# Performance work log

Hardware: AMD Instinct MI355X
Metric: run time of the kernel (lower is better)

## Reference

```python
import jax, jax.numpy as jnp
import numpy as np

BLK = 128            # weight_block_size for w8a16 blockwise dequant
H = 1024             # hidden_size
I = 512              # moe_intermediate_size
E = 64               # n_routed_experts
T = 512              # tokens (seq_len)
K = 6                # num_experts_per_tok
G = 8                # n_group
TG = 3               # topk_group
NSH = 2              # n_shared_experts
I2 = I * NSH         # shared expert intermediate size
ROUTED_SCALE = 2.5
NORM_TOPK = True


def dq(w_int8, scale, blk=BLK):
    """Blockwise w8a16 dequant: w [..., M, N] int8, scale [..., M/blk, N/blk] f32."""
    *lead, M, N = w_int8.shape
    w = w_int8.astype(scale.dtype).reshape(*lead, M // blk, blk, N // blk, blk)
    return (w * scale[..., :, None, :, None]).reshape(*lead, M, N)


def setup_inputs() -> dict:
    key = jax.random.key(0)
    ks = jax.random.split(key, 16)
    ri = lambda k, shp: jax.random.randint(k, shp, -8, 8, dtype=jnp.int8)
    rs = lambda k, shp: jax.random.uniform(k, shp, minval=0.01, maxval=0.03, dtype=jnp.float32)
    return {
        "x": jax.random.normal(ks[0], (T, H), jnp.float32),
        "gate_w": jax.random.normal(ks[1], (E, H), jnp.float32) * 0.02,  # router gate [E,H]
        "wg": ri(ks[2], (E, I, H)),  "sg": rs(ks[3], (E, I // BLK, H // BLK)),
        "wu": ri(ks[4], (E, I, H)),  "su": rs(ks[5], (E, I // BLK, H // BLK)),
        "wd": ri(ks[6], (E, I, H)),  "sd": rs(ks[7], (E, I // BLK, H // BLK)),  # down, transposed layout [I,H]
        "sh_wg": ri(ks[8], (I2, H)),  "sh_sg": rs(ks[9], (I2 // BLK, H // BLK)),
        "sh_wu": ri(ks[10], (I2, H)), "sh_su": rs(ks[11], (I2 // BLK, H // BLK)),
        "sh_wd": ri(ks[12], (I2, H)), "sh_sd": rs(ks[13], (I2 // BLK, H // BLK)),
    }


def _moe(x, gate_w, wg, sg, wu, su, wd, sd, sh_wg, sh_sg, sh_wu, sh_su, sh_wd, sh_sd):
    Tn = x.shape[0]
    # --- router: sigmoid scoring + group-limited top-k ---
    scores = jax.nn.sigmoid(x @ gate_w.T)                       # [T, E]
    gsz = E // G
    group_scores = scores.reshape(Tn, G, gsz).max(axis=-1)      # [T, G]
    _, gidx = jax.lax.top_k(group_scores, TG)                   # [T, TG]
    gmask = jax.nn.one_hot(gidx, G, dtype=scores.dtype).sum(1)  # [T, G]
    emask = jnp.repeat(gmask, gsz, axis=-1)                     # [T, E]
    masked = jnp.where(emask > 0, scores, -jnp.inf)
    w, idx = jax.lax.top_k(masked, K)                           # [T, K]
    if NORM_TOPK:
        w = w / (w.sum(-1, keepdims=True) + 1e-20)
    w = w * ROUTED_SCALE
    # per-token combine weights over experts
    comb = (jax.nn.one_hot(idx, E, dtype=x.dtype) * w[:, :, None]).sum(1)  # [T, E]

    # --- routed experts: dequantized silu-gated MLPs, masked dense combine ---
    Wg, Wu, Wd = dq(wg, sg), dq(wu, su), dq(wd, sd)             # [E, I, H]
    g = jnp.einsum('th,eih->eti', x, Wg)                        # [E, T, I]
    u = jnp.einsum('th,eih->eti', x, Wu)
    hmid = jax.nn.silu(g) * u
    y = jnp.einsum('eti,eih->eth', hmid, Wd)                    # [E, T, H]
    routed = jnp.einsum('eth,te->th', y, comb)                  # [T, H]

    # --- shared experts MLP ---
    Sg, Su, Sd = dq(sh_wg, sh_sg), dq(sh_wu, sh_su), dq(sh_wd, sh_sd)
    shared = (jax.nn.silu(x @ Sg.T) * (x @ Su.T)) @ Sd          # [T, H]
    return routed + shared


def reference(x, gate_w, wg, sg, wu, su, wd, sd, sh_wg, sh_sg, sh_wu, sh_su, sh_wd, sh_sd):
    return _moe(x, gate_w, wg, sg, wu, su, wd, sd,
                sh_wg, sh_sg, sh_wu, sh_su, sh_wd, sh_sd)
```

## Files before the change

### kernel.cpp

```cpp
#include <hip/hip_runtime.h>
#include <math.h>
#include <stdint.h>

#define T_   512
#define H_   1024
#define I_   512
#define E_   64
#define K_   6
#define G_   8
#define TG_  3
#define EB_  72

typedef _Float16 h8 __attribute__((ext_vector_type(8)));
typedef _Float16 h4v __attribute__((ext_vector_type(4)));
typedef float    f4 __attribute__((ext_vector_type(4)));

__global__ __launch_bounds__(64) void router_k(
    const float* __restrict__ x, const float* __restrict__ gw,
    int* __restrict__ cnt, int* __restrict__ tlist, float* __restrict__ wlist)
{
  const int t   = blockIdx.x;
  const int tid = threadIdx.x;
  __shared__ float sx[H_];
  __shared__ float sc[E_];

  for (int h4 = tid; h4 < H_/4; h4 += 64)
    ((float4*)sx)[h4] = ((const float4*)(x + (size_t)t*H_))[h4];
  __syncthreads();

  const float* wr = gw + (size_t)tid * H_;
  float acc = 0.f;
  for (int h = 0; h < H_; h += 4) {
    float4 xv = *(const float4*)(sx + h);
    float4 wv = *(const float4*)(wr + h);
    acc = fmaf(xv.x, wv.x, acc); acc = fmaf(xv.y, wv.y, acc);
    acc = fmaf(xv.z, wv.z, acc); acc = fmaf(xv.w, wv.w, acc);
  }
  sc[tid] = 1.f / (1.f + expf(-acc));
  __syncthreads();

  if (tid == 0) {
    float gs[G_];
    #pragma unroll
    for (int g = 0; g < G_; g++) {
      float m = sc[g*8];
      #pragma unroll
      for (int j = 1; j < 8; j++) m = fmaxf(m, sc[g*8+j]);
      gs[g] = m;
    }
    unsigned gp = 0;
    for (int r = 0; r < TG_; r++) {
      int best = 0; float bv = -1e30f;
      for (int g = 0; g < G_; g++)
        if (!((gp >> g) & 1) && gs[g] > bv) { bv = gs[g]; best = g; }
      gp |= 1u << best;
    }
    int   eidx[K_]; float ew[K_];
    unsigned long long em = 0ull;
    float wsum = 0.f;
    for (int r = 0; r < K_; r++) {
      int best = 0; float bv = -1e30f;
      for (int e = 0; e < E_; e++) {
        if (!((gp >> (e >> 3)) & 1)) continue;
        if ((em >> e) & 1ull) continue;
        if (sc[e] > bv) { bv = sc[e]; best = e; }
      }
      em |= 1ull << best; eidx[r] = best; ew[r] = bv; wsum += bv;
    }
    const float inv = 2.5f / (wsum + 1e-20f);
    for (int r = 0; r < K_; r++) {
      int e = eidx[r];
      int pos = atomicAdd(&cnt[e], 1);
      tlist[e*T_ + pos] = (t << 13) | (t*K_ + r);
      wlist[e*T_ + pos] = ew[r] * inv;
    }
  }
}

__global__ void pseudo_init_k(int* cnt, int* tlist, float* wlist) {
  int s = blockIdx.x*256 + threadIdx.x;
  if (s == 0) { cnt[64] = T_; cnt[65] = T_; }
  if (s < 1024) {
    int e = 64 + (s >> 9);
    int t = s & 511;
    tlist[e*T_ + t] = (t << 13) | (3072 + s);
    wlist[e*T_ + t] = 1.0f;
  }
}

__global__ __launch_bounds__(256) void xh_prep_k(
    const float* __restrict__ x, _Float16* __restrict__ xh)
{
  int i = blockIdx.x*256 + threadIdx.x;
  float4 v = ((const float4*)x)[i];
  h4v o = { (_Float16)v.x, (_Float16)v.y, (_Float16)v.z, (_Float16)v.w };
  *(h4v*)(xh + (size_t)i*4) = o;
}

__device__ __forceinline__ void eb_decode(int eb, const int* cnt,
                                          int& e, int& lo, int& hi) {
  if (eb < E_) { e = eb; lo = 0; hi = cnt[e]; }
  else { int q = (eb - E_) & 3; e = E_ + ((eb - E_) >> 2); lo = q*128; hi = lo + 128; }
}

__device__ __forceinline__ h8 bfrag(const int* __restrict__ p, float s) {
  int4 a = *(const int4*)(p);
  int4 b = *(const int4*)(p + 4);
  union { _Float16 f[8]; h8 v; } t;
  t.f[0]=(_Float16)((float)a.x*s); t.f[1]=(_Float16)((float)a.y*s);
  t.f[2]=(_Float16)((float)a.z*s); t.f[3]=(_Float16)((float)a.w*s);
  t.f[4]=(_Float16)((float)b.x*s); t.f[5]=(_Float16)((float)b.y*s);
  t.f[6]=(_Float16)((float)b.z*s); t.f[7]=(_Float16)((float)b.w*s);
  return t.v;
}

__global__ __launch_bounds__(256) void gateup_k(
    const _Float16* __restrict__ xh,
    const int* __restrict__ wg, const float* __restrict__ sg,
    const int* __restrict__ wu, const float* __restrict__ su,
    const int* __restrict__ shwg, const float* __restrict__ shsg,
    const int* __restrict__ shwu, const float* __restrict__ shsu,
    const int* __restrict__ cnt, const int* __restrict__ tlist,
    const float* __restrict__ wlist,
    _Float16* __restrict__ hmid)
{
  const int ic = blockIdx.x;
  const int eb = blockIdx.y;
  int e, lo, hi;
  eb_decode(eb, cnt, e, lo, hi);
  if (hi <= lo) return;

  const int tid  = threadIdx.x;
  const int lane = tid & 63;
  const int wv   = tid >> 6;
  const int mr   = lane & 15;
  const int quad = lane >> 4;

  const int *wgb, *wub; const float *sgp, *sup; int sib;
  if (e < E_) {
    wgb = wg + (size_t)e*I_*H_;  wub = wu + (size_t)e*I_*H_;
    sgp = sg + e*32;  sup = su + e*32;  sib = ic >> 1;
  } else {
    int hf = e - E_;
    wgb = shwg + (size_t)hf*512*H_;  wub = shwu + (size_t)hf*512*H_;
    sgp = shsg;  sup = shsu;  sib = hf*4 + (ic >> 1);
  }
  float scg[8], scu[8];
  #pragma unroll
  for (int hb = 0; hb < 8; hb++) { scg[hb] = sgp[sib*8+hb]; scu[hb] = sup[sib*8+hb]; }

  const int r0 = ic*64 + wv*16 + mr;
  const int* gp = wgb + (size_t)r0*H_;
  const int* up = wub + (size_t)r0*H_;

  __shared__ int   stok[64];
  __shared__ int   srow[64];
  __shared__ float swt[64];

  for (int base = lo; base < hi; base += 64) {
    __syncthreads();
    if (tid < 64) {
      int slot = base + tid;
      if (slot < hi) {
        int ent = tlist[e*T_ + slot];
        stok[tid] = ent >> 13; srow[tid] = ent & 8191; swt[tid] = wlist[e*T_ + slot];
      } else { stok[tid] = -1; srow[tid] = 0; swt[tid] = 0.f; }
    }
    __syncthreads();

    const _Float16* ax[4];
    #pragma unroll
    for (int mt = 0; mt < 4; mt++) {
      int tok = stok[mt*16 + mr];
      ax[mt] = xh + (size_t)(tok < 0 ? 0 : tok) * H_ + quad*8;
    }

    f4 accg[4], accu[4];
    #pragma unroll
    for (int mt = 0; mt < 4; mt++) { accg[mt] = (f4){0.f,0.f,0.f,0.f}; accu[mt] = accg[mt]; }

    #pragma unroll 4
    for (int kt = 0; kt < 32; kt++) {
      const int k0 = kt*32 + quad*8;
      const float sg_ = scg[kt>>2], su_ = scu[kt>>2];
      h8 bg = bfrag(gp + k0, sg_);
      h8 bu = bfrag(up + k0, su_);
      #pragma unroll
      for (int mt = 0; mt < 4; mt++) {
        h8 av = *(const h8*)(ax[mt] + kt*32);
        accg[mt] = __builtin_amdgcn_mfma_f32_16x16x32_f16(av, bg, accg[mt], 0,0,0);
        accu[mt] = __builtin_amdgcn_mfma_f32_16x16x32_f16(av, bu, accu[mt], 0,0,0);
      }
    }

    const int icol = ic*64 + wv*16 + mr;
    #pragma unroll
    for (int mt = 0; mt < 4; mt++) {
      #pragma unroll
      for (int r = 0; r < 4; r++) {
        int sl = mt*16 + quad*4 + r;
        if (stok[sl] >= 0) {
          float g = accg[mt][r];
          float m = g / (1.f + expf(-g)) * accu[mt][r] * swt[sl];
          hmid[(size_t)srow[sl]*I_ + icol] = (_Float16)m;
        }
      }
    }
  }
}

__global__ __launch_bounds__(256) void down_k(
    const int* __restrict__ wd, const float* __restrict__ sd,
    const int* __restrict__ shwd, const float* __restrict__ shsd,
    const int* __restrict__ cnt, const int* __restrict__ tlist,
    const _Float16* __restrict__ hmid, float* __restrict__ out)
{
  const int hc = blockIdx.x;
  const int eb = blockIdx.y;
  int e, lo, hi;
  eb_decode(eb, cnt, e, lo, hi);
  if (hi <= lo) return;

  const int tid  = threadIdx.x;
  const int lane = tid & 63;
  const int wv   = tid >> 6;
  const int mr   = lane & 15;
  const int quad = lane >> 4;

  const int* wb; const float* sdp; int sib0;
  if (e < E_) { wb = wd + (size_t)e*I_*H_;        sdp = sd + e*32;  sib0 = 0; }
  else { int hf = e - E_; wb = shwd + (size_t)hf*512*H_; sdp = shsd; sib0 = hf*4; }
  float scd[4];
  #pragma unroll
  for (int ib = 0; ib < 4; ib++) scd[ib] = sdp[(sib0+ib)*8 + hc];

  const int hcol0 = hc*128 + wv*32 + mr;
  const int* bcol0 = wb + hcol0;

  __shared__ int stok[64];
  __shared__ int srow[64];

  for (int base = lo; base < hi; base += 64) {
    __syncthreads();
    if (tid < 64) {
      int slot = base + tid;
      if (slot < hi) {
        int ent = tlist[e*T_ + slot];
        stok[tid] = ent >> 13; srow[tid] = ent & 8191;
      } else { stok[tid] = -1; srow[tid] = 0; }
    }
    __syncthreads();

    const _Float16* ap[4];
    #pragma unroll
    for (int mt = 0; mt < 4; mt++)
      ap[mt] = hmid + (size_t)srow[mt*16 + mr]*I_ + quad*8;

    f4 a0[4], a1[4];
    #pragma unroll
    for (int mt = 0; mt < 4; mt++) { a0[mt] = (f4){0.f,0.f,0.f,0.f}; a1[mt] = a0[mt]; }

    #pragma unroll 2
    for (int kt = 0; kt < 16; kt++) {
      const float s = scd[kt>>2];
      const size_t ib0 = (size_t)(kt*32 + quad*8) * H_;
      union { _Float16 f[8]; h8 v; } b0, b1;
      #pragma unroll
      for (int j = 0; j < 8; j++) {
        b0.f[j] = (_Float16)((float)bcol0[ib0 + (size_t)j*H_     ] * s);
        b1.f[j] = (_Float16)((float)bcol0[ib0 + (size_t)j*H_ + 16] * s);
      }
      #pragma unroll
      for (int mt = 0; mt < 4; mt++) {
        h8 av = *(const h8*)(ap[mt] + kt*32);
        a0[mt] = __builtin_amdgcn_mfma_f32_16x16x32_f16(av, b0.v, a0[mt], 0,0,0);
        a1[mt] = __builtin_amdgcn_mfma_f32_16x16x32_f16(av, b1.v, a1[mt], 0,0,0);
      }
    }

    #pragma unroll
    for (int mt = 0; mt < 4; mt++) {
      #pragma unroll
      for (int p = 0; p < 2; p++) {
        f4 av2 = (p == 0) ? a0[mt] : a1[mt];
        const int hcol = hcol0 + p*16;
        #pragma unroll
        for (int r = 0; r < 4; r++) {
          int sl = mt*16 + quad*4 + r;
          int t = stok[sl];
          if (t >= 0) atomicAdd(out + (size_t)t*H_ + hcol, av2[r]);
        }
      }
    }
  }
}

extern "C" void kernel_launch(void* const* d_in, const int* in_sizes, int n_in,
                              void* d_out, int out_size, void* d_ws, size_t ws_size,
                              hipStream_t stream) {
  (void)in_sizes; (void)n_in; (void)ws_size;
  const float* x    = (const float*)d_in[0];
  const float* gw   = (const float*)d_in[1];
  const int*   wg   = (const int*  )d_in[2];
  const float* sg   = (const float*)d_in[3];
  const int*   wu   = (const int*  )d_in[4];
  const float* su   = (const float*)d_in[5];
  const int*   wd   = (const int*  )d_in[6];
  const float* sd   = (const float*)d_in[7];
  const int*   shwg = (const int*  )d_in[8];
  const float* shsg = (const float*)d_in[9];
  const int*   shwu = (const int*  )d_in[10];
  const float* shsu = (const float*)d_in[11];
  const int*   shwd = (const int*  )d_in[12];
  const float* shsd = (const float*)d_in[13];
  float* out = (float*)d_out;

  char* ws = (char*)d_ws;
  int*      cnt   = (int*     ) ws;
  int*      tlist = (int*     )(ws + 1024);
  float*    wlist = (float*   )(ws + 1024 + 66*T_*4);
  _Float16* hmid  = (_Float16*)(ws + 1024 + 2*66*T_*4);
  _Float16* xh    = (_Float16*)(ws + 1024 + 2*66*T_*4 + 4096*I_*2);

  hipMemsetAsync(cnt, 0, 1024, stream);
  hipMemsetAsync(d_out, 0, (size_t)out_size * sizeof(float), stream);
  xh_prep_k<<<T_*H_/1024, 256, 0, stream>>>(x, xh);
  router_k<<<T_, 64, 0, stream>>>(x, gw, cnt, tlist, wlist);
  pseudo_init_k<<<4, 256, 0, stream>>>(cnt, tlist, wlist);
  gateup_k<<<dim3(8, EB_), 256, 0, stream>>>(xh, wg, sg, wu, su,
                                             shwg, shsg, shwu, shsu,
                                             cnt, tlist, wlist, hmid);
  down_k<<<dim3(8, EB_), 256, 0, stream>>>(wd, sd, shwd, shsd,
                                           cnt, tlist, hmid, out);
}
```

Baseline: 541.1 us.

## Double-buffer int weight tiles in LDS via async global_load_lds in gate/up and down

```diff
diff --git a/kernel.cpp b/kernel.cpp
--- a/kernel.cpp
+++ b/kernel.cpp
@@ -9,7 +9,7 @@
 #define K_   6
 #define G_   8
 #define TG_  3
-#define EB_  72
+#define EB_  80
 
 typedef _Float16 h8 __attribute__((ext_vector_type(8)));
 typedef _Float16 h4v __attribute__((ext_vector_type(4)));
@@ -100,12 +100,16 @@
 __device__ __forceinline__ void eb_decode(int eb, const int* cnt,
                                           int& e, int& lo, int& hi) {
   if (eb < E_) { e = eb; lo = 0; hi = cnt[e]; }
-  else { int q = (eb - E_) & 3; e = E_ + ((eb - E_) >> 2); lo = q*128; hi = lo + 128; }
-}
-
-__device__ __forceinline__ h8 bfrag(const int* __restrict__ p, float s) {
-  int4 a = *(const int4*)(p);
-  int4 b = *(const int4*)(p + 4);
+  else { int q = (eb - E_) & 7; e = E_ + ((eb - E_) >> 3); lo = q*64; hi = lo + 64; }
+}
+
+__device__ __forceinline__ void gld16(const int* g, void* l) {
+  __builtin_amdgcn_global_load_lds(
+      (const __attribute__((address_space(1))) void*)g,
+      (__attribute__((address_space(3))) void*)l, 16, 0, 0);
+}
+
+__device__ __forceinline__ h8 cvt8(int4 a, int4 b, float s) {
   union { _Float16 f[8]; h8 v; } t;
   t.f[0]=(_Float16)((float)a.x*s); t.f[1]=(_Float16)((float)a.y*s);
   t.f[2]=(_Float16)((float)a.z*s); t.f[3]=(_Float16)((float)a.w*s);
@@ -114,7 +118,13 @@
   return t.v;
 }
 
-__global__ __launch_bounds__(256) void gateup_k(
+#define PIPE_SYNC() do { \
+    asm volatile("s_waitcnt vmcnt(0)" ::: "memory"); \
+    __builtin_amdgcn_s_barrier(); \
+    __builtin_amdgcn_sched_barrier(0); } while (0)
+
+#define NKT_G 16
+__global__ __launch_bounds__(256, 2) void gateup_k(
     const _Float16* __restrict__ xh,
     const int* __restrict__ wg, const float* __restrict__ sg,
     const int* __restrict__ wu, const float* __restrict__ su,
@@ -145,17 +155,27 @@
     wgb = shwg + (size_t)hf*512*H_;  wub = shwu + (size_t)hf*512*H_;
     sgp = shsg;  sup = shsu;  sib = hf*4 + (ic >> 1);
   }
-  float scg[8], scu[8];
-  #pragma unroll
-  for (int hb = 0; hb < 8; hb++) { scg[hb] = sgp[sib*8+hb]; scu[hb] = sup[sib*8+hb]; }
-
-  const int r0 = ic*64 + wv*16 + mr;
-  const int* gp = wgb + (size_t)r0*H_;
-  const int* up = wub + (size_t)r0*H_;
-
+  const int r0base = ic*64;
+
+  __shared__ int   ldsw[2][2][4096];
   __shared__ int   stok[64];
   __shared__ int   srow[64];
   __shared__ float swt[64];
+
+  auto stage = [&](int buf, int kt) {
+    const int k0 = kt * 64;
+    #pragma unroll
+    for (int i = 0; i < 4; i++) {
+      const int rl  = i*16 + wv*4 + (lane >> 4);
+      const int csw = (lane & 15) ^ (rl & 7);
+      const size_t go = (size_t)(r0base + rl)*H_ + k0 + csw*4;
+      gld16(wgb + go, &ldsw[buf][0][(i*16 + wv*4)*64]);
+      gld16(wub + go, &ldsw[buf][1][(i*16 + wv*4)*64]);
+    }
+  };
+
+  const int rr = wv*16 + mr;
+  const int sw = rr & 7;
 
   for (int base = lo; base < hi; base += 64) {
     __syncthreads();
@@ -179,21 +199,43 @@
     #pragma unroll
     for (int mt = 0; mt < 4; mt++) { accg[mt] = (f4){0.f,0.f,0.f,0.f}; accu[mt] = accg[mt]; }
 
-    #pragma unroll 4
-    for (int kt = 0; kt < 32; kt++) {
-      const int k0 = kt*32 + quad*8;
-      const float sg_ = scg[kt>>2], su_ = scu[kt>>2];
-      h8 bg = bfrag(gp + k0, sg_);
-      h8 bu = bfrag(up + k0, su_);
+    stage(0, 0);
+    PIPE_SYNC();
+
+    int cur = 0;
+    for (int kt = 0; kt < NKT_G; kt++) {
+      h8 avv[4][2];
       #pragma unroll
       for (int mt = 0; mt < 4; mt++) {
-        h8 av = *(const h8*)(ax[mt] + kt*32);
-        accg[mt] = __builtin_amdgcn_mfma_f32_16x16x32_f16(av, bg, accg[mt], 0,0,0);
-        accu[mt] = __builtin_amdgcn_mfma_f32_16x16x32_f16(av, bu, accu[mt], 0,0,0);
-      }
-    }
-
-    const int icol = ic*64 + wv*16 + mr;
+        avv[mt][0] = *(const h8*)(ax[mt] + kt*64);
+        avv[mt][1] = *(const h8*)(ax[mt] + kt*64 + 32);
+      }
+      __builtin_amdgcn_sched_barrier(0);
+      if (kt < NKT_G-1) stage(cur ^ 1, kt + 1);
+
+      const float sg_ = sgp[sib*8 + (kt >> 1)];
+      const float su_ = sup[sib*8 + (kt >> 1)];
+      const int* lg = &ldsw[cur][0][0];
+      const int* lu = &ldsw[cur][1][0];
+      #pragma unroll
+      for (int ktl = 0; ktl < 2; ktl++) {
+        const int c0 = ktl*8 + quad*2;
+        int4 g0 = *(const int4*)(lg + rr*64 + (( c0   ) ^ sw)*4);
+        int4 g1 = *(const int4*)(lg + rr*64 + (((c0+1)) ^ sw)*4);
+        int4 u0 = *(const int4*)(lu + rr*64 + (( c0   ) ^ sw)*4);
+        int4 u1 = *(const int4*)(lu + rr*64 + (((c0+1)) ^ sw)*4);
+        h8 bg = cvt8(g0, g1, sg_);
+        h8 bu = cvt8(u0, u1, su_);
+        #pragma unroll
+        for (int mt = 0; mt < 4; mt++) {
+          accg[mt] = __builtin_amdgcn_mfma_f32_16x16x32_f16(avv[mt][ktl], bg, accg[mt], 0,0,0);
+          accu[mt] = __builtin_amdgcn_mfma_f32_16x16x32_f16(avv[mt][ktl], bu, accu[mt], 0,0,0);
+        }
+      }
+      if (kt < NKT_G-1) { PIPE_SYNC(); cur ^= 1; }
+    }
+
+    const int icol = ic*64 + rr;
     #pragma unroll
     for (int mt = 0; mt < 4; mt++) {
       #pragma unroll
@@ -209,7 +251,8 @@
   }
 }
 
-__global__ __launch_bounds__(256) void down_k(
+#define NKT_D 8
+__global__ __launch_bounds__(256, 2) void down_k(
     const int* __restrict__ wd, const float* __restrict__ sd,
     const int* __restrict__ shwd, const float* __restrict__ shsd,
     const int* __restrict__ cnt, const int* __restrict__ tlist,
@@ -230,15 +273,28 @@
   const int* wb; const float* sdp; int sib0;
   if (e < E_) { wb = wd + (size_t)e*I_*H_;        sdp = sd + e*32;  sib0 = 0; }
   else { int hf = e - E_; wb = shwd + (size_t)hf*512*H_; sdp = shsd; sib0 = hf*4; }
-  float scd[4];
-  #pragma unroll
-  for (int ib = 0; ib < 4; ib++) scd[ib] = sdp[(sib0+ib)*8 + hc];
-
-  const int hcol0 = hc*128 + wv*32 + mr;
-  const int* bcol0 = wb + hcol0;
-
+
+  __shared__ int ldsd[2][8192];
   __shared__ int stok[64];
   __shared__ int srow[64];
+
+  auto stage = [&](int buf, int kt) {
+    const int i0 = kt*64;
+    #pragma unroll
+    for (int s = 0; s < 8; s++) {
+      const int rl  = s*8 + wv*2 + (lane >> 5);
+      const int csw = (lane & 31) ^ (((rl >> 3) & 1) << 2);
+      gld16(wb + (size_t)(i0 + rl)*H_ + hc*128 + csw*4,
+            &ldsd[buf][(s*8 + wv*2)*128]);
+    }
+  };
+
+  const int hcol0 = hc*128 + wv*32 + mr;
+  const int swd   = (quad & 1) << 2;
+  const int cd0   = wv*32 + mr;
+  const int cd1   = cd0 + 16;
+  const int off0  = (((cd0 >> 2) ^ swd) << 2) + (cd0 & 3);
+  const int off1  = (((cd1 >> 2) ^ swd) << 2) + (cd1 & 3);
 
   for (int base = lo; base < hi; base += 64) {
     __syncthreads();
@@ -260,22 +316,38 @@
     #pragma unroll
     for (int mt = 0; mt < 4; mt++) { a0[mt] = (f4){0.f,0.f,0.f,0.f}; a1[mt] = a0[mt]; }
 
-    #pragma unroll 2
-    for (int kt = 0; kt < 16; kt++) {
-      const float s = scd[kt>>2];
-      const size_t ib0 = (size_t)(kt*32 + quad*8) * H_;
-      union { _Float16 f[8]; h8 v; } b0, b1;
-      #pragma unroll
-      for (int j = 0; j < 8; j++) {
-        b0.f[j] = (_Float16)((float)bcol0[ib0 + (size_t)j*H_     ] * s);
-        b1.f[j] = (_Float16)((float)bcol0[ib0 + (size_t)j*H_ + 16] * s);
-      }
+    stage(0, 0);
+    PIPE_SYNC();
+
+    int cur = 0;
+    for (int kt = 0; kt < NKT_D; kt++) {
+      h8 avv[4][2];
       #pragma unroll
       for (int mt = 0; mt < 4; mt++) {
-        h8 av = *(const h8*)(ap[mt] + kt*32);
-        a0[mt] = __builtin_amdgcn_mfma_f32_16x16x32_f16(av, b0.v, a0[mt], 0,0,0);
-        a1[mt] = __builtin_amdgcn_mfma_f32_16x16x32_f16(av, b1.v, a1[mt], 0,0,0);
-      }
+        avv[mt][0] = *(const h8*)(ap[mt] + kt*64);
+        avv[mt][1] = *(const h8*)(ap[mt] + kt*64 + 32);
+      }
+      __builtin_amdgcn_sched_barrier(0);
+      if (kt < NKT_D-1) stage(cur ^ 1, kt + 1);
+
+      const float s = sdp[(sib0 + (kt >> 1))*8 + hc];
+      const int* lb = &ldsd[cur][0];
+      #pragma unroll
+      for (int ktl = 0; ktl < 2; ktl++) {
+        union { _Float16 f[8]; h8 v; } b0, b1;
+        #pragma unroll
+        for (int j = 0; j < 8; j++) {
+          const int r = ktl*32 + quad*8 + j;
+          b0.f[j] = (_Float16)((float)lb[r*128 + off0] * s);
+          b1.f[j] = (_Float16)((float)lb[r*128 + off1] * s);
+        }
+        #pragma unroll
+        for (int mt = 0; mt < 4; mt++) {
+          a0[mt] = __builtin_amdgcn_mfma_f32_16x16x32_f16(avv[mt][ktl], b0.v, a0[mt], 0,0,0);
+          a1[mt] = __builtin_amdgcn_mfma_f32_16x16x32_f16(avv[mt][ktl], b1.v, a1[mt], 0,0,0);
+        }
+      }
+      if (kt < NKT_D-1) { PIPE_SYNC(); cur ^= 1; }
     }
 
     #pragma unroll
```

Measured after the change: 517.2 us. 4.4% less time.

## Stage dequantized weights through LDS with software pipelining and replace atomics with scratch combine

Applied to the files above, without the earlier changes.

```diff
diff --git a/kernel.cpp b/kernel.cpp
--- a/kernel.cpp
+++ b/kernel.cpp
@@ -9,7 +9,7 @@
 #define K_   6
 #define G_   8
 #define TG_  3
-#define EB_  72
+#define EB_  80
 
 typedef _Float16 h8 __attribute__((ext_vector_type(8)));
 typedef _Float16 h4v __attribute__((ext_vector_type(4)));
@@ -100,21 +100,53 @@
 __device__ __forceinline__ void eb_decode(int eb, const int* cnt,
                                           int& e, int& lo, int& hi) {
   if (eb < E_) { e = eb; lo = 0; hi = cnt[e]; }
-  else { int q = (eb - E_) & 3; e = E_ + ((eb - E_) >> 2); lo = q*128; hi = lo + 128; }
-}
-
-__device__ __forceinline__ h8 bfrag(const int* __restrict__ p, float s) {
-  int4 a = *(const int4*)(p);
-  int4 b = *(const int4*)(p + 4);
+  else { int q = (eb - E_) & 7; e = E_ + ((eb - E_) >> 3); lo = q*64; hi = lo + 64; }
+}
+
+__device__ __forceinline__ h8 cvt8i(int4 a, int4 b) {
   union { _Float16 f[8]; h8 v; } t;
-  t.f[0]=(_Float16)((float)a.x*s); t.f[1]=(_Float16)((float)a.y*s);
-  t.f[2]=(_Float16)((float)a.z*s); t.f[3]=(_Float16)((float)a.w*s);
-  t.f[4]=(_Float16)((float)b.x*s); t.f[5]=(_Float16)((float)b.y*s);
-  t.f[6]=(_Float16)((float)b.z*s); t.f[7]=(_Float16)((float)b.w*s);
+  t.f[0]=(_Float16)a.x; t.f[1]=(_Float16)a.y; t.f[2]=(_Float16)a.z; t.f[3]=(_Float16)a.w;
+  t.f[4]=(_Float16)b.x; t.f[5]=(_Float16)b.y; t.f[6]=(_Float16)b.z; t.f[7]=(_Float16)b.w;
   return t.v;
 }
 
-__global__ __launch_bounds__(256) void gateup_k(
+#define NKT_G 16
+
+#define GU_STEP(KT, WN)                                                       \
+  do {                                                                        \
+    asm volatile("s_waitcnt vmcnt(" #WN ") lgkmcnt(0)" ::: "memory");         \
+    __builtin_amdgcn_sched_barrier(0);                                        \
+    __builtin_amdgcn_s_barrier();                                             \
+    if ((KT) + 1 < NKT_G)                                                     \
+      *(h8*)(wdst + (((KT)+1)&1)*4608) =                                      \
+          cvt8i(Wr[((KT)+1)%3][0], Wr[((KT)+1)%3][1]);                        \
+    if ((KT) + 3 < NKT_G) {                                                   \
+      Wr[((KT)+3)%3][0] = *(const int4*)(wsrc + ((KT)+3)*64);                 \
+      Wr[((KT)+3)%3][1] = *(const int4*)(wsrc + ((KT)+3)*64 + 4);             \
+    }                                                                         \
+    {                                                                         \
+      const char* tb = tb0 + (((KT)&1))*4608;                                 \
+      h8 bg0 = *(const h8*)(tb);                                              \
+      h8 bg1 = *(const h8*)(tb + 64);                                         \
+      h8 bu0 = *(const h8*)(tb + 2304);                                       \
+      h8 bu1 = *(const h8*)(tb + 2304 + 64);                                  \
+      if (((KT)&1) == 0) { partg = (f4){0.f,0.f,0.f,0.f}; partu = partg; }    \
+      partg = __builtin_amdgcn_mfma_f32_16x16x32_f16(Ar[(KT)%3][0], bg0, partg, 0,0,0); \
+      partg = __builtin_amdgcn_mfma_f32_16x16x32_f16(Ar[(KT)%3][1], bg1, partg, 0,0,0); \
+      partu = __builtin_amdgcn_mfma_f32_16x16x32_f16(Ar[(KT)%3][0], bu0, partu, 0,0,0); \
+      partu = __builtin_amdgcn_mfma_f32_16x16x32_f16(Ar[(KT)%3][1], bu1, partu, 0,0,0); \
+      if (((KT)&1) == 1) {                                                    \
+        totg += partg * sgv[(KT)>>1];                                         \
+        totu += partu * suv[(KT)>>1];                                         \
+      }                                                                       \
+    }                                                                         \
+    if ((KT) + 3 < NKT_G) {                                                   \
+      Ar[((KT)+3)%3][0] = *(const h8*)(ax + ((KT)+3)*64);                     \
+      Ar[((KT)+3)%3][1] = *(const h8*)(ax + ((KT)+3)*64 + 32);                \
+    }                                                                         \
+  } while (0)
+
+__global__ __launch_bounds__(256, 6) void gateup_k(
     const _Float16* __restrict__ xh,
     const int* __restrict__ wg, const float* __restrict__ sg,
     const int* __restrict__ wu, const float* __restrict__ su,
@@ -139,23 +171,28 @@
   const int *wgb, *wub; const float *sgp, *sup; int sib;
   if (e < E_) {
     wgb = wg + (size_t)e*I_*H_;  wub = wu + (size_t)e*I_*H_;
-    sgp = sg + e*32;  sup = su + e*32;  sib = ic >> 1;
+    sgp = sg + e*32;  sup = su + e*32;  sib = ic >> 3;
   } else {
     int hf = e - E_;
     wgb = shwg + (size_t)hf*512*H_;  wub = shwu + (size_t)hf*512*H_;
-    sgp = shsg;  sup = shsu;  sib = hf*4 + (ic >> 1);
-  }
-  float scg[8], scu[8];
+    sgp = shsg;  sup = shsu;  sib = hf*4 + (ic >> 3);
+  }
+  float sgv[8], suv[8];
   #pragma unroll
-  for (int hb = 0; hb < 8; hb++) { scg[hb] = sgp[sib*8+hb]; scu[hb] = sup[sib*8+hb]; }
-
-  const int r0 = ic*64 + wv*16 + mr;
-  const int* gp = wgb + (size_t)r0*H_;
-  const int* up = wub + (size_t)r0*H_;
-
-  __shared__ int   stok[64];
-  __shared__ int   srow[64];
-  __shared__ float swt[64];
+  for (int b = 0; b < 8; b++) { sgv[b] = sgp[sib*8+b]; suv[b] = sup[sib*8+b]; }
+
+  __shared__ _Float16 tile[2][2][16][72];
+  __shared__ int stok[64]; __shared__ int srw[64]; __shared__ float swt[64];
+  char* tilebytes = (char*)&tile[0][0][0][0];
+
+  const int smat = wv >> 1;
+  const int srow = (wv & 1)*8 + (lane >> 3);
+  const int* wsrc = (smat ? wub : wgb) + (size_t)(ic*16 + srow)*H_ + (lane & 7)*8;
+  char* wdst = tilebytes + smat*2304 + srow*144 + (lane & 7)*16;
+  const char* tb0 = tilebytes + mr*144 + quad*16;
+
+  int4 Wr[3][2];
+  h8   Ar[3][2];
 
   for (int base = lo; base < hi; base += 64) {
     __syncthreads();
@@ -163,57 +200,98 @@
       int slot = base + tid;
       if (slot < hi) {
         int ent = tlist[e*T_ + slot];
-        stok[tid] = ent >> 13; srow[tid] = ent & 8191; swt[tid] = wlist[e*T_ + slot];
-      } else { stok[tid] = -1; srow[tid] = 0; swt[tid] = 0.f; }
+        stok[tid] = ent >> 13; srw[tid] = ent & 8191; swt[tid] = wlist[e*T_ + slot];
+      } else { stok[tid] = -1; srw[tid] = 0; swt[tid] = 0.f; }
     }
     __syncthreads();
 
-    const _Float16* ax[4];
+    int tk = stok[wv*16 + mr]; if (tk < 0) tk = 0;
+    const _Float16* ax = xh + (size_t)tk*H_ + quad*8;
+
+    f4 totg = (f4){0.f,0.f,0.f,0.f}, totu = totg, partg = totg, partu = totg;
+
+    Wr[0][0] = *(const int4*)(wsrc);       Wr[0][1] = *(const int4*)(wsrc + 4);
+    Ar[0][0] = *(const h8*)(ax);           Ar[0][1] = *(const h8*)(ax + 32);
+    Wr[1][0] = *(const int4*)(wsrc + 64);  Wr[1][1] = *(const int4*)(wsrc + 68);
+    Ar[1][0] = *(const h8*)(ax + 64);      Ar[1][1] = *(const h8*)(ax + 96);
+    Wr[2][0] = *(const int4*)(wsrc + 128); Wr[2][1] = *(const int4*)(wsrc + 132);
+    Ar[2][0] = *(const h8*)(ax + 128);     Ar[2][1] = *(const h8*)(ax + 160);
+    *(h8*)(wdst) = cvt8i(Wr[0][0], Wr[0][1]);
+
+    GU_STEP(0,6);  GU_STEP(1,6);  GU_STEP(2,6);  GU_STEP(3,6);
+    GU_STEP(4,6);  GU_STEP(5,6);  GU_STEP(6,6);  GU_STEP(7,6);
+    GU_STEP(8,6);  GU_STEP(9,6);  GU_STEP(10,6); GU_STEP(11,6);
+    GU_STEP(12,6); GU_STEP(13,6); GU_STEP(14,2); GU_STEP(15,0);
+
+    const int icol = ic*16 + mr;
     #pragma unroll
-    for (int mt = 0; mt < 4; mt++) {
-      int tok = stok[mt*16 + mr];
-      ax[mt] = xh + (size_t)(tok < 0 ? 0 : tok) * H_ + quad*8;
-    }
-
-    f4 accg[4], accu[4];
-    #pragma unroll
-    for (int mt = 0; mt < 4; mt++) { accg[mt] = (f4){0.f,0.f,0.f,0.f}; accu[mt] = accg[mt]; }
-
-    #pragma unroll 4
-    for (int kt = 0; kt < 32; kt++) {
-      const int k0 = kt*32 + quad*8;
-      const float sg_ = scg[kt>>2], su_ = scu[kt>>2];
-      h8 bg = bfrag(gp + k0, sg_);
-      h8 bu = bfrag(up + k0, su_);
-      #pragma unroll
-      for (int mt = 0; mt < 4; mt++) {
-        h8 av = *(const h8*)(ax[mt] + kt*32);
-        accg[mt] = __builtin_amdgcn_mfma_f32_16x16x32_f16(av, bg, accg[mt], 0,0,0);
-        accu[mt] = __builtin_amdgcn_mfma_f32_16x16x32_f16(av, bu, accu[mt], 0,0,0);
+    for (int r = 0; r < 4; r++) {
+      int sl = wv*16 + quad*4 + r;
+      if (stok[sl] >= 0) {
+        float g = totg[r];
+        float m = g / (1.f + expf(-g)) * totu[r] * swt[sl];
+        hmid[(size_t)srw[sl]*I_ + icol] = (_Float16)m;
       }
     }
-
-    const int icol = ic*64 + wv*16 + mr;
-    #pragma unroll
-    for (int mt = 0; mt < 4; mt++) {
-      #pragma unroll
-      for (int r = 0; r < 4; r++) {
-        int sl = mt*16 + quad*4 + r;
-        if (stok[sl] >= 0) {
-          float g = accg[mt][r];
-          float m = g / (1.f + expf(-g)) * accu[mt][r] * swt[sl];
-          hmid[(size_t)srow[sl]*I_ + icol] = (_Float16)m;
-        }
-      }
-    }
-  }
-}
-
-__global__ __launch_bounds__(256) void down_k(
+  }
+}
+#undef GU_STEP
+
+#define NKT_D 8
+
+#define DN_LDW(S, KT)                                                         \
+  do {                                                                        \
+    Wr[S][0] = *(const int2*)(dsrc + (size_t)((KT)*64 + 0)*H_);               \
+    Wr[S][1] = *(const int2*)(dsrc + (size_t)((KT)*64 + 1)*H_);               \
+    Wr[S][2] = *(const int2*)(dsrc + (size_t)((KT)*64 + 2)*H_);               \
+    Wr[S][3] = *(const int2*)(dsrc + (size_t)((KT)*64 + 3)*H_);               \
+  } while (0)
+
+#define DN_WRITE(S, BUF)                                                      \
+  do {                                                                        \
+    union { _Float16 f[4]; h4v v; } v0, v1;                                   \
+    v0.f[0]=(_Float16)Wr[S][0].x; v0.f[1]=(_Float16)Wr[S][1].x;               \
+    v0.f[2]=(_Float16)Wr[S][2].x; v0.f[3]=(_Float16)Wr[S][3].x;               \
+    v1.f[0]=(_Float16)Wr[S][0].y; v1.f[1]=(_Float16)Wr[S][1].y;               \
+    v1.f[2]=(_Float16)Wr[S][2].y; v1.f[3]=(_Float16)Wr[S][3].y;               \
+    *(h4v*)(ddst + (BUF)*4608)       = v0.v;                                  \
+    *(h4v*)(ddst + (BUF)*4608 + 144) = v1.v;                                  \
+  } while (0)
+
+#define DN_STEP(KT, WN)                                                       \
+  do {                                                                        \
+    asm volatile("s_waitcnt vmcnt(" #WN ") lgkmcnt(0)" ::: "memory");         \
+    __builtin_amdgcn_sched_barrier(0);                                        \
+    __builtin_amdgcn_s_barrier();                                             \
+    if ((KT) + 1 < NKT_D) DN_WRITE(((KT)+1)%3, ((KT)+1)&1);                   \
+    if ((KT) + 3 < NKT_D) DN_LDW(((KT)+3)%3, (KT)+3);                         \
+    {                                                                         \
+      const char* tb = tb0 + (((KT)&1))*4608;                                 \
+      h8 b00 = *(const h8*)(tb);                                              \
+      h8 b01 = *(const h8*)(tb + 64);                                         \
+      h8 b10 = *(const h8*)(tb + 2304);                                       \
+      h8 b11 = *(const h8*)(tb + 2304 + 64);                                  \
+      if (((KT)&1) == 0) { part0 = (f4){0.f,0.f,0.f,0.f}; part1 = part0; }    \
+      part0 = __builtin_amdgcn_mfma_f32_16x16x32_f16(Ar[(KT)%3][0], b00, part0, 0,0,0); \
+      part0 = __builtin_amdgcn_mfma_f32_16x16x32_f16(Ar[(KT)%3][1], b01, part0, 0,0,0); \
+      part1 = __builtin_amdgcn_mfma_f32_16x16x32_f16(Ar[(KT)%3][0], b10, part1, 0,0,0); \
+      part1 = __builtin_amdgcn_mfma_f32_16x16x32_f16(Ar[(KT)%3][1], b11, part1, 0,0,0); \
+      if (((KT)&1) == 1) {                                                    \
+        tot0 += part0 * sdv[(KT)>>1];                                         \
+        tot1 += part1 * sdv[(KT)>>1];                                         \
+      }                                                                       \
+    }                                                                         \
+    if ((KT) + 3 < NKT_D) {                                                   \
+      Ar[((KT)+3)%3][0] = *(const h8*)(ap + ((KT)+3)*64);                     \
+      Ar[((KT)+3)%3][1] = *(const h8*)(ap + ((KT)+3)*64 + 32);                \
+    }                                                                         \
+  } while (0)
+
+__global__ __launch_bounds__(256, 6) void down_k(
     const int* __restrict__ wd, const float* __restrict__ sd,
     const int* __restrict__ shwd, const float* __restrict__ shsd,
     const int* __restrict__ cnt, const int* __restrict__ tlist,
-    const _Float16* __restrict__ hmid, float* __restrict__ out)
+    const _Float16* __restrict__ hmid, float* __restrict__ scr)
 {
   const int hc = blockIdx.x;
   const int eb = blockIdx.y;
@@ -230,15 +308,21 @@
   const int* wb; const float* sdp; int sib0;
   if (e < E_) { wb = wd + (size_t)e*I_*H_;        sdp = sd + e*32;  sib0 = 0; }
   else { int hf = e - E_; wb = shwd + (size_t)hf*512*H_; sdp = shsd; sib0 = hf*4; }
-  float scd[4];
+  float sdv[4];
   #pragma unroll
-  for (int ib = 0; ib < 4; ib++) scd[ib] = sdp[(sib0+ib)*8 + hc];
-
-  const int hcol0 = hc*128 + wv*32 + mr;
-  const int* bcol0 = wb + hcol0;
-
-  __shared__ int stok[64];
-  __shared__ int srow[64];
+  for (int ib = 0; ib < 4; ib++) sdv[ib] = sdp[(sib0+ib)*8 + (hc >> 2)];
+
+  __shared__ _Float16 tile[2][32][72];
+  __shared__ int stok[64]; __shared__ int srw[64];
+  char* tilebytes = (char*)&tile[0][0][0];
+
+  const int rg = lane >> 4;
+  const int* dsrc = wb + (size_t)(wv*16 + rg*4)*H_ + hc*32 + (lane & 15)*2;
+  char* ddst = tilebytes + ((lane & 15)*2)*144 + (wv*16 + rg*4)*2;
+  const char* tb0 = tilebytes + mr*144 + quad*16;
+
+  int2 Wr[3][4];
+  h8   Ar[3][2];
 
   for (int base = lo; base < hi; base += 64) {
     __syncthreads();
@@ -246,59 +330,64 @@
       int slot = base + tid;
       if (slot < hi) {
         int ent = tlist[e*T_ + slot];
-        stok[tid] = ent >> 13; srow[tid] = ent & 8191;
-      } else { stok[tid] = -1; srow[tid] = 0; }
+        stok[tid] = ent >> 13; srw[tid] = ent & 8191;
+      } else { stok[tid] = -1; srw[tid] = 0; }
     }
     __syncthreads();
 
-    const _Float16* ap[4];
+    const _Float16* ap = hmid + (size_t)srw[wv*16 + mr]*I_ + quad*8;
+
+    f4 tot0 = (f4){0.f,0.f,0.f,0.f}, tot1 = tot0, part0 = tot0, part1 = tot0;
+
+    DN_LDW(0, 0);
+    Ar[0][0] = *(const h8*)(ap);        Ar[0][1] = *(const h8*)(ap + 32);
+    DN_LDW(1, 1);
+    Ar[1][0] = *(const h8*)(ap + 64);   Ar[1][1] = *(const h8*)(ap + 96);
+    DN_LDW(2, 2);
+    Ar[2][0] = *(const h8*)(ap + 128);  Ar[2][1] = *(const h8*)(ap + 160);
+    DN_WRITE(0, 0);
+
+    DN_STEP(0,6); DN_STEP(1,6); DN_STEP(2,6); DN_STEP(3,6);
+    DN_STEP(4,6); DN_STEP(5,6); DN_STEP(6,2); DN_STEP(7,0);
+
     #pragma unroll
-    for (int mt = 0; mt < 4; mt++)
-      ap[mt] = hmid + (size_t)srow[mt*16 + mr]*I_ + quad*8;
-
-    f4 a0[4], a1[4];
-    #pragma unroll
-    for (int mt = 0; mt < 4; mt++) { a0[mt] = (f4){0.f,0.f,0.f,0.f}; a1[mt] = a0[mt]; }
-
-    #pragma unroll 2
-    for (int kt = 0; kt < 16; kt++) {
-      const float s = scd[kt>>2];
-      const size_t ib0 = (size_t)(kt*32 + quad*8) * H_;
-      union { _Float16 f[8]; h8 v; } b0, b1;
-      #pragma unroll
-      for (int j = 0; j < 8; j++) {
-        b0.f[j] = (_Float16)((float)bcol0[ib0 + (size_t)j*H_     ] * s);
-        b1.f[j] = (_Float16)((float)bcol0[ib0 + (size_t)j*H_ + 16] * s);
+    for (int r = 0; r < 4; r++) {
+      int sl = wv*16 + quad*4 + r;
+      if (stok[sl] >= 0) {
+        int t  = stok[sl];
+        int sr = srw[sl];
+        int rank = (sr < 3072) ? (sr - t*6) : (6 + ((sr - 3072) >> 9));
+        float* dst = scr + (size_t)(t*8 + rank)*H_ + hc*32 + mr;
+        dst[0]  = tot0[r];
+        dst[16] = tot1[r];
       }
-      #pragma unroll
-      for (int mt = 0; mt < 4; mt++) {
-        h8 av = *(const h8*)(ap[mt] + kt*32);
-        a0[mt] = __builtin_amdgcn_mfma_f32_16x16x32_f16(av, b0.v, a0[mt], 0,0,0);
-        a1[mt] = __builtin_amdgcn_mfma_f32_16x16x32_f16(av, b1.v, a1[mt], 0,0,0);
-      }
-    }
-
-    #pragma unroll
-    for (int mt = 0; mt < 4; mt++) {
-      #pragma unroll
-      for (int p = 0; p < 2; p++) {
-        f4 av2 = (p == 0) ? a0[mt] : a1[mt];
-        const int hcol = hcol0 + p*16;
-        #pragma unroll
-        for (int r = 0; r < 4; r++) {
-          int sl = mt*16 + quad*4 + r;
-          int t = stok[sl];
-          if (t >= 0) atomicAdd(out + (size_t)t*H_ + hcol, av2[r]);
-        }
-      }
-    }
-  }
+    }
+  }
+}
+#undef DN_STEP
+#undef DN_WRITE
+#undef DN_LDW
+
+__global__ __launch_bounds__(256) void combine_k(
+    const float* __restrict__ scr, float* __restrict__ out)
+{
+  int i = blockIdx.x*256 + threadIdx.x;
+  int t = i >> 8;
+  int c = i & 255;
+  const float4* base = (const float4*)(scr + (size_t)t*8*H_) + c;
+  float4 s = base[0];
+  #pragma unroll
+  for (int r = 1; r < 8; r++) {
+    float4 v = base[(size_t)r*(H_/4)];
+    s.x += v.x; s.y += v.y; s.z += v.z; s.w += v.w;
+  }
+  ((float4*)out)[i] = s;
 }
 
 extern "C" void kernel_launch(void* const* d_in, const int* in_sizes, int n_in,
                               void* d_out, int out_size, void* d_ws, size_t ws_size,
                               hipStream_t stream) {
-  (void)in_sizes; (void)n_in; (void)ws_size;
+  (void)in_sizes; (void)n_in; (void)ws_size; (void)out_size;
   const float* x    = (const float*)d_in[0];
   const float* gw   = (const float*)d_in[1];
   const int*   wg   = (const int*  )d_in[2];
@@ -321,15 +410,16 @@
   float*    wlist = (float*   )(ws + 1024 + 66*T_*4);
   _Float16* hmid  = (_Float16*)(ws + 1024 + 2*66*T_*4);
   _Float16* xh    = (_Float16*)(ws + 1024 + 2*66*T_*4 + 4096*I_*2);
+  float*    scr   = (float*   )(ws + 1024 + 2*66*T_*4 + 4096*I_*2 + T_*H_*2);
 
   hipMemsetAsync(cnt, 0, 1024, stream);
-  hipMemsetAsync(d_out, 0, (size_t)out_size * sizeof(float), stream);
   xh_prep_k<<<T_*H_/1024, 256, 0, stream>>>(x, xh);
   router_k<<<T_, 64, 0, stream>>>(x, gw, cnt, tlist, wlist);
   pseudo_init_k<<<4, 256, 0, stream>>>(cnt, tlist, wlist);
-  gateup_k<<<dim3(8, EB_), 256, 0, stream>>>(xh, wg, sg, wu, su,
-                                             shwg, shsg, shwu, shsu,
-                                             cnt, tlist, wlist, hmid);
-  down_k<<<dim3(8, EB_), 256, 0, stream>>>(wd, sd, shwd, shsd,
-                                           cnt, tlist, hmid, out);
-}
+  gateup_k<<<dim3(32, EB_), 256, 0, stream>>>(xh, wg, sg, wu, su,
+                                              shwg, shsg, shwu, shsu,
+                                              cnt, tlist, wlist, hmid);
+  down_k<<<dim3(32, EB_), 256, 0, stream>>>(wd, sd, shwd, shsd,
+                                            cnt, tlist, hmid, scr);
+  combine_k<<<T_*H_/1024, 256, 0, stream>>>(scr, out);
+}
```

New measurement: 593.4 us. 1.1x slower.
